# Performance work log

Hardware: AMD Instinct MI355X
Metric: run time of the kernel (lower is better)

Reference implementation:

```python
import jax, jax.numpy as jnp
import numpy as np

N_NODES = 100000
EPS = 1e-5  # BatchNorm1d default eps


def gcn_conv(x, W, b, row, col, n):
    """PyG GCNConv: add self-loops, symmetric normalization, linear, scatter-add."""
    loop = jnp.arange(n, dtype=row.dtype)
    row_f = jnp.concatenate([row, loop])  # sources
    col_f = jnp.concatenate([col, loop])  # targets
    # degree of target nodes (edge_weight = 1)
    deg = jax.ops.segment_sum(jnp.ones_like(col_f, dtype=x.dtype), col_f, num_segments=n)
    dinv = jnp.where(deg > 0, jax.lax.rsqrt(deg), 0.0)
    norm = dinv[row_f] * dinv[col_f]  # [E+N]
    h = x @ W  # [N, out]
    msg = h[row_f] * norm[:, None]  # [E+N, out]
    out = jax.ops.segment_sum(msg, col_f, num_segments=n)
    return out + b


def batch_norm(x, gamma, beta):
    # training-mode BatchNorm1d: biased batch stats over node axis
    mean = jnp.mean(x, axis=0)
    var = jnp.var(x, axis=0)
    return (x - mean) * jax.lax.rsqrt(var + EPS) * gamma + beta


def setup_inputs() -> dict:
    key = jax.random.key(0)
    ks = jax.random.split(key, 8)
    n, e, f_in, h = N_NODES, 1600000, 25, 128
    x = jax.random.normal(ks[0], (n, f_in), dtype=jnp.float32)
    edge_index = jax.random.randint(ks[1], (2, e), 0, n, dtype=jnp.int64)
    s1 = 1.0 / np.sqrt(f_in)
    s2 = 1.0 / np.sqrt(h)
    W1 = jax.random.uniform(ks[2], (f_in, h), jnp.float32, -s1, s1)
    b1 = jax.random.uniform(ks[3], (h,), jnp.float32, -s1, s1)
    gamma = jnp.ones((h,), jnp.float32)
    beta = jnp.zeros((h,), jnp.float32)
    W2 = jax.random.uniform(ks[4], (h, h), jnp.float32, -s2, s2)
    b2 = jax.random.uniform(ks[5], (h,), jnp.float32, -s2, s2)
    return {"x": x, "edge_index": edge_index, "W1": W1, "b1": b1,
            "gamma": gamma, "beta": beta, "W2": W2, "b2": b2}


def reference(x, edge_index, W1, b1, gamma, beta, W2, b2):
    row, col = edge_index[0], edge_index[1]
    n = x.shape[0]
    h = jax.nn.relu(gcn_conv(x, W1, b1, row, col, n))
    h = batch_norm(h, gamma, beta)
    h = jax.nn.relu(gcn_conv(h, W2, b2, row, col, n))
    return h
```

## Files before the change

### kernel.cpp

```cpp
#include <hip/hip_runtime.h>
#include <stdint.h>


#define HID 128
#define NBB 512

typedef short bf16x8 __attribute__((ext_vector_type(8)));
typedef float f32x4 __attribute__((ext_vector_type(4)));

__device__ __forceinline__ unsigned short f2bf(float f) {
    unsigned int u = __float_as_uint(f);
    unsigned int r = (u + 0x7FFFu + ((u >> 16) & 1u)) >> 16;
    return (unsigned short)r;
}
__device__ __forceinline__ unsigned int pack2bf(float lo, float hi) {
    return (unsigned int)f2bf(lo) | ((unsigned int)f2bf(hi) << 16);
}
__device__ __forceinline__ float bflo(unsigned int v) { return __uint_as_float(v << 16); }
__device__ __forceinline__ float bfhi(unsigned int v) { return __uint_as_float(v & 0xffff0000u); }

__global__ void detect_kernel(const unsigned int* __restrict__ w, int* __restrict__ mode, int nwords) {
    __shared__ int any;
    if (threadIdx.x == 0) any = 0;
    __syncthreads();
    for (int i = threadIdx.x * 2 + 1; i < nwords && i < 8192; i += 512) {
        if (w[i] != 0) atomicOr(&any, 1);
    }
    __syncthreads();
    if (threadIdx.x == 0) *mode = any ? 0 : 1;
}

__device__ __forceinline__ int load_idx(const void* ei, size_t i, int mode) {
    return mode ? (int)((const long long*)ei)[i] : ((const int*)ei)[i];
}

__global__ __launch_bounds__(256) void count_q_kernel(const void* __restrict__ ei,
                                                      const int* __restrict__ modep,
                                                      int* __restrict__ qcnt,
                                                      int E, int CHUNK, int nchunk) {
    __shared__ int qc[512];
    for (int i = threadIdx.x; i < nchunk; i += 256) qc[i] = 0;
    __syncthreads();
    int mode = *modep;
    int beg = blockIdx.x * CHUNK;
    int end = beg + CHUNK; if (end > E) end = E;
    for (int e = beg + threadIdx.x; e < end; e += 256) {
        int c = load_idx(ei, (size_t)E + e, mode);
        atomicAdd(&qc[c >> 8], 1);
    }
    __syncthreads();
    for (int i = threadIdx.x; i < nchunk; i += 256)
        qcnt[blockIdx.x * nchunk + i] = qc[i];
}

__global__ __launch_bounds__(256) void scanq_partial_kernel(const int* __restrict__ qcnt,
                                                            int* __restrict__ blocksum,
                                                            int NQ, int nchunk) {
    int j0 = blockIdx.x * 2048 + threadIdx.x * 8;
    int s = 0;
    #pragma unroll
    for (int i = 0; i < 8; ++i) {
        int j = j0 + i;
        if (j < NQ) {
            int q = j >> 9, b = j & (NBB - 1);
            s += qcnt[b * nchunk + q];
        }
    }
    #pragma unroll
    for (int off = 32; off > 0; off >>= 1) s += __shfl_down(s, off);
    __shared__ int ls[4];
    if ((threadIdx.x & 63) == 0) ls[threadIdx.x >> 6] = s;
    __syncthreads();
    if (threadIdx.x == 0) blocksum[blockIdx.x] = ls[0] + ls[1] + ls[2] + ls[3];
}

__global__ __launch_bounds__(1024) void scanq_blocksums_kernel(const int* __restrict__ blocksum,
                                                               int* __restrict__ blockoff,
                                                               int* __restrict__ qoff,
                                                               int nsb, int NQ) {
    __shared__ int s[1024];
    int t = threadIdx.x;
    int own = (t < nsb) ? blocksum[t] : 0;
    s[t] = own;
    __syncthreads();
    for (int off = 1; off < 1024; off <<= 1) {
        int v = s[t] + ((t >= off) ? s[t - off] : 0);
        __syncthreads();
        s[t] = v;
        __syncthreads();
    }
    if (t < nsb) blockoff[t] = s[t] - own;
    if (t == 1023) qoff[NQ] = s[1023];
}

__global__ __launch_bounds__(256) void scanq_finalize_kernel(const int* __restrict__ qcnt,
                                                             const int* __restrict__ blockoff,
                                                             int* __restrict__ qoff,
                                                             int NQ, int nchunk) {
    int t = threadIdx.x;
    int j0 = blockIdx.x * 2048 + t * 8;
    int v[8], own = 0;
    #pragma unroll
    for (int i = 0; i < 8; ++i) {
        int j = j0 + i;
        v[i] = 0;
        if (j < NQ) {
            int q = j >> 9, b = j & (NBB - 1);
            v[i] = qcnt[b * nchunk + q];
        }
        own += v[i];
    }
    __shared__ int s[256];
    s[t] = own;
    __syncthreads();
    for (int off = 1; off < 256; off <<= 1) {
        int x = s[t] + ((t >= off) ? s[t - off] : 0);
        __syncthreads();
        s[t] = x;
        __syncthreads();
    }
    int e = blockoff[blockIdx.x] + s[t] - own;
    #pragma unroll
    for (int i = 0; i < 8; ++i) {
        int j = j0 + i;
        if (j < NQ) qoff[j] = e;
        e += v[i];
    }
}

__global__ __launch_bounds__(256) void bin_kernel(const void* __restrict__ ei,
                                                  const int* __restrict__ modep,
                                                  const int* __restrict__ qoff,
                                                  unsigned int* __restrict__ packed,
                                                  int E, int CHUNK, int nchunk) {
    __shared__ int cur[512];
    for (int i = threadIdx.x; i < nchunk; i += 256)
        cur[i] = qoff[i * NBB + blockIdx.x];
    __syncthreads();
    int mode = *modep;
    int beg = blockIdx.x * CHUNK;
    int end = beg + CHUNK; if (end > E) end = E;
    for (int e = beg + threadIdx.x; e < end; e += 256) {
        int c = load_idx(ei, (size_t)E + e, mode);
        int r = load_idx(ei, (size_t)e, mode);
        int pos = atomicAdd(&cur[c >> 8], 1);
        packed[pos] = ((unsigned)(c & 255) << 24) | (unsigned)r;
    }
}

__global__ __launch_bounds__(256) void chunk_build_kernel(
    const unsigned int* __restrict__ packed, const int* __restrict__ qoff,
    int* __restrict__ rowptr, float* __restrict__ dinv,
    int* __restrict__ edge_src, int n, int E) {
    int q = blockIdx.x;
    int t = threadIdx.x;
    int pbeg = qoff[q * NBB];
    int pend = qoff[(q + 1) * NBB];
    __shared__ int cnt256[256], cur[256], s[256];
    cnt256[t] = 0;
    __syncthreads();
    for (int i = pbeg + t; i < pend; i += 256)
        atomicAdd(&cnt256[packed[i] >> 24], 1);
    __syncthreads();
    int own = cnt256[t];
    s[t] = own;
    __syncthreads();
    for (int off = 1; off < 256; off <<= 1) {
        int x = s[t] + ((t >= off) ? s[t - off] : 0);
        __syncthreads();
        s[t] = x;
        __syncthreads();
    }
    int pref = s[t] - own;
    int node = (q << 8) + t;
    if (node < n) {
        rowptr[node] = pbeg + pref;
        dinv[node] = rsqrtf((float)(own + 1));
    }
    cur[t] = pbeg + pref;
    if (q == gridDim.x - 1 && t == 0) rowptr[n] = E;
    __syncthreads();
    for (int i = pbeg + t; i < pend; i += 256) {
        unsigned int u = packed[i];
        int pos = atomicAdd(&cur[u >> 24], 1);
        edge_src[pos] = (int)(u & 0xFFFFFFu);
    }
}

__global__ __launch_bounds__(256) void xpad_kernel(const float* __restrict__ x,
                                                   unsigned int* __restrict__ xp, int n) {
    int r = blockIdx.x * 256 + threadIdx.x;
    if (r >= n) return;
    const float* xr = x + (size_t)r * 25;
    unsigned int* o = xp + (size_t)r * 16;
    #pragma unroll
    for (int j = 0; j < 12; ++j)
        o[j] = pack2bf(xr[j * 2], xr[j * 2 + 1]);
    o[12] = pack2bf(xr[24], 0.f);
    o[13] = 0u; o[14] = 0u; o[15] = 0u;
}

__global__ __launch_bounds__(256) void l1_kernel(
    const unsigned int* __restrict__ xp, const int* __restrict__ rowptr,
    const int* __restrict__ edge_src, const float* __restrict__ dinv,
    const float* __restrict__ W, const float* __restrict__ bias,
    unsigned short* __restrict__ y1, float* __restrict__ bnsum,
    float* __restrict__ bnsumsq, int n) {
    __shared__ float lw[25 * HID];
    __shared__ float lb[HID];
    for (int i = threadIdx.x; i < 25 * HID; i += 256) lw[i] = W[i];
    if (threadIdx.x < HID) lb[threadIdx.x] = bias[threadIdx.x];
    __syncthreads();
    int lane = threadIdx.x & 63;
    int g = lane >> 4, i = lane & 15;
    int wid0 = (blockIdx.x * 256 + threadIdx.x) >> 6;
    float s0 = 0.f, q0 = 0.f, s1 = 0.f, q1 = 0.f;
    for (int node = wid0; node < n; node += 4096) {
        int beg = rowptr[node], end = rowptr[node + 1];
        float dc = dinv[node];
        float ax = 0.f, ay = 0.f;
        for (int b = beg; b < end; b += 64) {
            int m = end - b; if (m > 64) m = 64;
            int s = 0; float w = 0.f;
            if (lane < m) { s = edge_src[b + lane]; w = dinv[s]; }
            int nsteps = (m + 3) >> 2;
            for (int t = 0; t < nsteps; ++t) {
                int e = 4 * t + g;
                int sj = __shfl(s, e);
                float wj = __shfl(w, e);
                unsigned int u = xp[(size_t)sj * 16 + i];
                ax = fmaf(bflo(u), wj, ax);
                ay = fmaf(bfhi(u), wj, ay);
            }
        }
        if (g == 0) {
            unsigned int u = xp[(size_t)node * 16 + i];
            ax = fmaf(bflo(u), dc, ax);
            ay = fmaf(bfhi(u), dc, ay);
        }
        ax += __shfl_xor(ax, 16); ax += __shfl_xor(ax, 32);
        ay += __shfl_xor(ay, 16); ay += __shfl_xor(ay, 32);
        ax *= dc; ay *= dc;
        float acc0 = lb[lane], acc1 = lb[lane + 64];
        #pragma unroll
        for (int k = 0; k < 25; ++k) {
            float yk = (k & 1) ? __shfl(ay, k >> 1) : __shfl(ax, k >> 1);
            acc0 = fmaf(yk, lw[k * HID + lane], acc0);
            acc1 = fmaf(yk, lw[k * HID + lane + 64], acc1);
        }
        acc0 = fmaxf(acc0, 0.f);
        acc1 = fmaxf(acc1, 0.f);
        y1[(size_t)node * HID + lane] = f2bf(acc0);
        y1[(size_t)node * HID + lane + 64] = f2bf(acc1);
        s0 += acc0; q0 = fmaf(acc0, acc0, q0);
        s1 += acc1; q1 = fmaf(acc1, acc1, q1);
    }
    __shared__ float r0[256], r1[256], r2[256], r3[256];
    r0[threadIdx.x] = s0; r1[threadIdx.x] = q0;
    r2[threadIdx.x] = s1; r3[threadIdx.x] = q1;
    __syncthreads();
    if (threadIdx.x < 64) {
        int l = threadIdx.x;
        float a = r0[l] + r0[l + 64] + r0[l + 128] + r0[l + 192];
        float b = r1[l] + r1[l + 64] + r1[l + 128] + r1[l + 192];
        float c = r2[l] + r2[l + 64] + r2[l + 128] + r2[l + 192];
        float d = r3[l] + r3[l + 64] + r3[l + 128] + r3[l + 192];
        atomicAdd(&bnsum[l], a);
        atomicAdd(&bnsumsq[l], b);
        atomicAdd(&bnsum[l + 64], c);
        atomicAdd(&bnsumsq[l + 64], d);
    }
}

__global__ __launch_bounds__(256) void propagate_kernel(
    const unsigned short* __restrict__ h, const int* __restrict__ rowptr,
    const int* __restrict__ edge_src, const float* __restrict__ dinv,
    const float* __restrict__ bias, float* __restrict__ out, int n) {
    int wid = (blockIdx.x * 256 + threadIdx.x) >> 6;
    if (wid >= n) return;
    int lane = threadIdx.x & 63;
    int beg = rowptr[wid], end = rowptr[wid + 1];
    float dc = dinv[wid];
    float ax = 0.f, ay = 0.f;
    const unsigned int* hp = (const unsigned int*)h;
    for (int b = beg; b < end; b += 64) {
        int m = end - b; if (m > 64) m = 64;
        int s = 0; float w = 0.f;
        if (lane < m) { s = edge_src[b + lane]; w = dinv[s]; }
        for (int j = 0; j < m; j += 8) {
            int s0 = __shfl(s, j + 0), s1 = __shfl(s, j + 1);
            int s2 = __shfl(s, j + 2), s3 = __shfl(s, j + 3);
            int s4 = __shfl(s, j + 4), s5 = __shfl(s, j + 5);
            int s6 = __shfl(s, j + 6), s7 = __shfl(s, j + 7);
            unsigned int v0 = hp[(size_t)s0 * 64 + lane];
            unsigned int v1 = hp[(size_t)s1 * 64 + lane];
            unsigned int v2 = hp[(size_t)s2 * 64 + lane];
            unsigned int v3 = hp[(size_t)s3 * 64 + lane];
            unsigned int v4 = hp[(size_t)s4 * 64 + lane];
            unsigned int v5 = hp[(size_t)s5 * 64 + lane];
            unsigned int v6 = hp[(size_t)s6 * 64 + lane];
            unsigned int v7 = hp[(size_t)s7 * 64 + lane];
            float w0 = __shfl(w, j + 0), w1 = __shfl(w, j + 1);
            float w2 = __shfl(w, j + 2), w3 = __shfl(w, j + 3);
            float w4 = __shfl(w, j + 4), w5 = __shfl(w, j + 5);
            float w6 = __shfl(w, j + 6), w7 = __shfl(w, j + 7);
            ax = fmaf(bflo(v0), w0, ax); ay = fmaf(bfhi(v0), w0, ay);
            ax = fmaf(bflo(v1), w1, ax); ay = fmaf(bfhi(v1), w1, ay);
            ax = fmaf(bflo(v2), w2, ax); ay = fmaf(bfhi(v2), w2, ay);
            ax = fmaf(bflo(v3), w3, ax); ay = fmaf(bfhi(v3), w3, ay);
            ax = fmaf(bflo(v4), w4, ax); ay = fmaf(bfhi(v4), w4, ay);
            ax = fmaf(bflo(v5), w5, ax); ay = fmaf(bfhi(v5), w5, ay);
            ax = fmaf(bflo(v6), w6, ax); ay = fmaf(bfhi(v6), w6, ay);
            ax = fmaf(bflo(v7), w7, ax); ay = fmaf(bfhi(v7), w7, ay);
        }
    }
    {
        unsigned int v = hp[(size_t)wid * 64 + lane];
        ax = fmaf(bflo(v), dc, ax);
        ay = fmaf(bfhi(v), dc, ay);
    }
    float bx = bias[lane * 2], by = bias[lane * 2 + 1];
    ax = fmaxf(fmaf(ax, dc, bx), 0.f);
    ay = fmaxf(fmaf(ay, dc, by), 0.f);
    *(float2*)(out + (size_t)wid * HID + lane * 2) = make_float2(ax, ay);
}

__global__ void bn_finalize_kernel(const float* __restrict__ sum, const float* __restrict__ sumsq,
                                   const float* __restrict__ gamma, const float* __restrict__ beta,
                                   float* __restrict__ scale, float* __restrict__ shift, float inv_n) {
    int c = threadIdx.x;
    float mean = sum[c] * inv_n;
    float var = sumsq[c] * inv_n - mean * mean;
    float sc = gamma[c] * rsqrtf(var + 1e-5f);
    scale[c] = sc;
    shift[c] = beta[c] - mean * sc;
}

__global__ __launch_bounds__(256) void wt_kernel(const float* __restrict__ W,
                                                 unsigned short* __restrict__ Wt) {
    int idx = blockIdx.x * 256 + threadIdx.x;
    int c = idx >> 7, k = idx & 127;
    Wt[c * 128 + k] = f2bf(W[k * 128 + c]);
}

__global__ __launch_bounds__(256) void gemm2_mfma_kernel(
    const unsigned short* __restrict__ yb, const unsigned short* __restrict__ Wt,
    const float* __restrict__ scale, const float* __restrict__ shift,
    unsigned short* __restrict__ out, int n) {
    __shared__ unsigned short lwt[128 * 136];
    __shared__ unsigned short ly[128 * 136];
    int t = threadIdx.x;
    int base = blockIdx.x * 128;

    {
        const unsigned int* w32 = (const unsigned int*)Wt;
        unsigned int* l32 = (unsigned int*)lwt;
        #pragma unroll
        for (int i = 0; i < 32; ++i) {
            int idx = t + i * 256;
            int r = idx >> 6, cp = idx & 63;
            l32[r * 68 + cp] = w32[r * 64 + cp];
        }
    }
    {
        int r = t >> 1, hh = t & 1;
        int gr = base + r;
        unsigned int* l32 = (unsigned int*)ly;
        const uint4* yrow = (const uint4*)(yb + (size_t)gr * HID + hh * 64);
        #pragma unroll
        for (int j = 0; j < 8; ++j) {
            uint4 u = make_uint4(0u, 0u, 0u, 0u);
            if (gr < n) u = yrow[j];
            int gk = hh * 64 + j * 8;
            float a0 = fmaf(bflo(u.x), scale[gk + 0], shift[gk + 0]);
            float a1 = fmaf(bfhi(u.x), scale[gk + 1], shift[gk + 1]);
            float a2 = fmaf(bflo(u.y), scale[gk + 2], shift[gk + 2]);
            float a3 = fmaf(bfhi(u.y), scale[gk + 3], shift[gk + 3]);
            float a4 = fmaf(bflo(u.z), scale[gk + 4], shift[gk + 4]);
            float a5 = fmaf(bfhi(u.z), scale[gk + 5], shift[gk + 5]);
            float a6 = fmaf(bflo(u.w), scale[gk + 6], shift[gk + 6]);
            float a7 = fmaf(bfhi(u.w), scale[gk + 7], shift[gk + 7]);
            l32[r * 68 + hh * 32 + j * 4 + 0] = pack2bf(a0, a1);
            l32[r * 68 + hh * 32 + j * 4 + 1] = pack2bf(a2, a3);
            l32[r * 68 + hh * 32 + j * 4 + 2] = pack2bf(a4, a5);
            l32[r * 68 + hh * 32 + j * 4 + 3] = pack2bf(a6, a7);
        }
    }
    __syncthreads();

    int w = t >> 6, lane = t & 63;
    int li = lane & 15, lg = lane >> 4;
    f32x4 acc[2][8];
    #pragma unroll
    for (int a = 0; a < 2; ++a)
        #pragma unroll
        for (int b = 0; b < 8; ++b) acc[a][b] = (f32x4){0.f, 0.f, 0.f, 0.f};

    #pragma unroll
    for (int ks = 0; ks < 4; ++ks) {
        int kb = ks * 32 + lg * 8;
        bf16x8 af[2], bfr[8];
        #pragma unroll
        for (int rt = 0; rt < 2; ++rt)
            af[rt] = *(const bf16x8*)&ly[(w * 32 + rt * 16 + li) * 136 + kb];
        #pragma unroll
        for (int cf = 0; cf < 8; ++cf)
            bfr[cf] = *(const bf16x8*)&lwt[(cf * 16 + li) * 136 + kb];
        #pragma unroll
        for (int rt = 0; rt < 2; ++rt)
            #pragma unroll
            for (int cf = 0; cf < 8; ++cf)
                acc[rt][cf] = __builtin_amdgcn_mfma_f32_16x16x32_bf16(
                    af[rt], bfr[cf], acc[rt][cf], 0, 0, 0);
    }

    #pragma unroll
    for (int rt = 0; rt < 2; ++rt) {
        #pragma unroll
        for (int reg = 0; reg < 4; ++reg) {
            int gr = base + w * 32 + rt * 16 + lg * 4 + reg;
            if (gr < n) {
                #pragma unroll
                for (int cf = 0; cf < 8; ++cf)
                    out[(size_t)gr * HID + cf * 16 + li] = f2bf(acc[rt][cf][reg]);
            }
        }
    }
}

extern "C" void kernel_launch(void* const* d_in, const int* in_sizes, int n_in,
                              void* d_out, int out_size, void* d_ws, size_t ws_size,
                              hipStream_t stream) {
    const float* x     = (const float*)d_in[0];
    const void*  ei    = d_in[1];
    const float* W1    = (const float*)d_in[2];
    const float* b1    = (const float*)d_in[3];
    const float* gamma = (const float*)d_in[4];
    const float* beta  = (const float*)d_in[5];
    const float* W2    = (const float*)d_in[6];
    const float* b2    = (const float*)d_in[7];
    float* out = (float*)d_out;

    const int f_in = 25;
    int n = in_sizes[0] / f_in;
    int E = in_sizes[1] / 2;
    int nchunk = (n + 255) >> 8;
    int NQ = nchunk * NBB;
    int nsb = (NQ + 2047) / 2048;
    int CHUNK = (E + NBB - 1) / NBB;

    char* ws = (char*)d_ws;
    size_t off = 0;
    auto alloc = [&](size_t bytes) -> void* {
        void* p = ws + off;
        off += (bytes + 511) & ~(size_t)511;
        return p;
    };
    int*   rowptr    = (int*)alloc(((size_t)n + 1) * 4);
    float* dinv      = (float*)alloc((size_t)n * 4);
    int*   edge_src  = (int*)alloc((size_t)E * 4);
    unsigned int* packed = (unsigned int*)alloc((size_t)E * 4);
    int*   qcnt      = (int*)alloc((size_t)NQ * 4);
    int*   qoff      = (int*)alloc(((size_t)NQ + 1) * 4);
    int*   blocksum  = (int*)alloc((size_t)nsb * 4);
    int*   blockoff  = (int*)alloc((size_t)nsb * 4);
    float* bnacc     = (float*)alloc(256 * 4);
    float* sclshift  = (float*)alloc(256 * 4);
    int*   mode      = (int*)alloc(4);
    unsigned int* xp   = (unsigned int*)alloc((size_t)n * 16 * 4);
    unsigned short* y1 = (unsigned short*)alloc((size_t)n * HID * 2);
    unsigned short* Wt = (unsigned short*)alloc(128 * 128 * 2);
    unsigned short* h  = (unsigned short*)alloc((size_t)n * HID * 2);

    hipMemsetAsync(bnacc, 0, 256 * 4, stream);

    detect_kernel<<<1, 256, 0, stream>>>((const unsigned int*)ei, mode, 2 * E);
    count_q_kernel<<<NBB, 256, 0, stream>>>(ei, mode, qcnt, E, CHUNK, nchunk);
    scanq_partial_kernel<<<nsb, 256, 0, stream>>>(qcnt, blocksum, NQ, nchunk);
    scanq_blocksums_kernel<<<1, 1024, 0, stream>>>(blocksum, blockoff, qoff, nsb, NQ);
    scanq_finalize_kernel<<<nsb, 256, 0, stream>>>(qcnt, blockoff, qoff, NQ, nchunk);
    bin_kernel<<<NBB, 256, 0, stream>>>(ei, mode, qoff, packed, E, CHUNK, nchunk);
    chunk_build_kernel<<<nchunk, 256, 0, stream>>>(packed, qoff, rowptr, dinv, edge_src, n, E);

    xpad_kernel<<<(n + 255) / 256, 256, 0, stream>>>(x, xp, n);
    l1_kernel<<<1024, 256, 0, stream>>>(xp, rowptr, edge_src, dinv, W1, b1,
                                        y1, bnacc, bnacc + 128, n);

    bn_finalize_kernel<<<1, 128, 0, stream>>>(bnacc, bnacc + 128, gamma, beta,
                                              sclshift, sclshift + 128, 1.0f / (float)n);

    wt_kernel<<<64, 256, 0, stream>>>(W2, Wt);
    gemm2_mfma_kernel<<<(n + 127) / 128, 256, 0, stream>>>(y1, Wt, sclshift, sclshift + 128, h, n);
    propagate_kernel<<<(n + 3) / 4, 256, 0, stream>>>(h, rowptr, edge_src, dinv, b2, out, n);
}
```

Measured before the change: 255.5 us.

## Process four nodes per wavefront in layer-1 aggregation with unrolled gathers

Restructures the layer-1 kernel so each wavefront handles four nodes at once, one per 16-lane group, instead of one node per wave. Each group walks its own edge list with four gathers unrolled per step, and the shuffle-based edge staging and cross-group reduction are gone. The dense 25x128 transform now gives each lane 8 output columns, written as one 16-byte store. BN statistics are reduced through shared-memory atomics, and the grid doubles to 2048 blocks. The cost is divergence: groups in a wave loop up to the largest degree among their four nodes, and per-lane register use rises.

```diff
diff --git a/kernel.cpp b/kernel.cpp
--- a/kernel.cpp
+++ b/kernel.cpp
@@ -208,67 +208,103 @@
     float* __restrict__ bnsumsq, int n) {
     __shared__ float lw[25 * HID];
     __shared__ float lb[HID];
-    for (int i = threadIdx.x; i < 25 * HID; i += 256) lw[i] = W[i];
-    if (threadIdx.x < HID) lb[threadIdx.x] = bias[threadIdx.x];
+    __shared__ float lsum[HID], lsq[HID];
+    for (int idx = threadIdx.x; idx < 25 * HID; idx += 256) lw[idx] = W[idx];
+    if (threadIdx.x < HID) {
+        lb[threadIdx.x] = bias[threadIdx.x];
+        lsum[threadIdx.x] = 0.f;
+        lsq[threadIdx.x] = 0.f;
+    }
     __syncthreads();
     int lane = threadIdx.x & 63;
-    int g = lane >> 4, i = lane & 15;
-    int wid0 = (blockIdx.x * 256 + threadIdx.x) >> 6;
-    float s0 = 0.f, q0 = 0.f, s1 = 0.f, q1 = 0.f;
-    for (int node = wid0; node < n; node += 4096) {
-        int beg = rowptr[node], end = rowptr[node + 1];
-        float dc = dinv[node];
+    int g = lane >> 4;
+    int i = lane & 15;
+    int wid = (blockIdx.x * 256 + threadIdx.x) >> 6;
+    int nwaves = gridDim.x << 2;
+    float psum[8], psq[8];
+    #pragma unroll
+    for (int j = 0; j < 8; ++j) { psum[j] = 0.f; psq[j] = 0.f; }
+
+    for (int base = 4 * wid; base < n; base += 4 * nwaves) {
+        int node = base + g;
+        bool act = node < n;
+        int nd = act ? node : 0;
+        int beg = rowptr[nd];
+        int end = act ? rowptr[nd + 1] : beg;
+        float dc = dinv[nd];
+        int deg = end - beg;
+        int md = deg;
+        md = max(md, __shfl_xor(md, 16));
+        md = max(md, __shfl_xor(md, 32));
         float ax = 0.f, ay = 0.f;
-        for (int b = beg; b < end; b += 64) {
-            int m = end - b; if (m > 64) m = 64;
-            int s = 0; float w = 0.f;
-            if (lane < m) { s = edge_src[b + lane]; w = dinv[s]; }
-            int nsteps = (m + 3) >> 2;
-            for (int t = 0; t < nsteps; ++t) {
-                int e = 4 * t + g;
-                int sj = __shfl(s, e);
-                float wj = __shfl(w, e);
-                unsigned int u = xp[(size_t)sj * 16 + i];
-                ax = fmaf(bflo(u), wj, ax);
-                ay = fmaf(bfhi(u), wj, ay);
-            }
-        }
-        if (g == 0) {
-            unsigned int u = xp[(size_t)node * 16 + i];
-            ax = fmaf(bflo(u), dc, ax);
-            ay = fmaf(bfhi(u), dc, ay);
-        }
-        ax += __shfl_xor(ax, 16); ax += __shfl_xor(ax, 32);
-        ay += __shfl_xor(ay, 16); ay += __shfl_xor(ay, 32);
+        for (int off = 0; off < md; off += 4) {
+            int e0 = beg + off, e1 = e0 + 1, e2 = e0 + 2, e3 = e0 + 3;
+            bool v0 = e0 < end, v1 = e1 < end, v2 = e2 < end, v3 = e3 < end;
+            int c0 = v0 ? e0 : 0, c1 = v1 ? e1 : 0;
+            int c2 = v2 ? e2 : 0, c3 = v3 ? e3 : 0;
+            int s0 = edge_src[c0];
+            int s1 = edge_src[c1];
+            int s2 = edge_src[c2];
+            int s3 = edge_src[c3];
+            unsigned int u0 = xp[(size_t)s0 * 16 + i];
+            unsigned int u1 = xp[(size_t)s1 * 16 + i];
+            unsigned int u2 = xp[(size_t)s2 * 16 + i];
+            unsigned int u3 = xp[(size_t)s3 * 16 + i];
+            float w0 = v0 ? dinv[s0] : 0.f;
+            float w1 = v1 ? dinv[s1] : 0.f;
+            float w2 = v2 ? dinv[s2] : 0.f;
+            float w3 = v3 ? dinv[s3] : 0.f;
+            ax = fmaf(bflo(u0), w0, ax); ay = fmaf(bfhi(u0), w0, ay);
+            ax = fmaf(bflo(u1), w1, ax); ay = fmaf(bfhi(u1), w1, ay);
+            ax = fmaf(bflo(u2), w2, ax); ay = fmaf(bfhi(u2), w2, ay);
+            ax = fmaf(bflo(u3), w3, ax); ay = fmaf(bfhi(u3), w3, ay);
+        }
+        {
+            unsigned int u = xp[(size_t)nd * 16 + i];
+            float ws = act ? dc : 0.f;
+            ax = fmaf(bflo(u), ws, ax);
+            ay = fmaf(bfhi(u), ws, ay);
+        }
         ax *= dc; ay *= dc;
-        float acc0 = lb[lane], acc1 = lb[lane + 64];
+        float acc[8];
+        #pragma unroll
+        for (int j = 0; j < 8; ++j) acc[j] = lb[i * 8 + j];
         #pragma unroll
         for (int k = 0; k < 25; ++k) {
-            float yk = (k & 1) ? __shfl(ay, k >> 1) : __shfl(ax, k >> 1);
-            acc0 = fmaf(yk, lw[k * HID + lane], acc0);
-            acc1 = fmaf(yk, lw[k * HID + lane + 64], acc1);
-        }
-        acc0 = fmaxf(acc0, 0.f);
-        acc1 = fmaxf(acc1, 0.f);
-        y1[(size_t)node * HID + lane] = f2bf(acc0);
-        y1[(size_t)node * HID + lane + 64] = f2bf(acc1);
-        s0 += acc0; q0 = fmaf(acc0, acc0, q0);
-        s1 += acc1; q1 = fmaf(acc1, acc1, q1);
-    }
-    __shared__ float r0[256], r1[256], r2[256], r3[256];
-    r0[threadIdx.x] = s0; r1[threadIdx.x] = q0;
-    r2[threadIdx.x] = s1; r3[threadIdx.x] = q1;
-    __syncthreads();
-    if (threadIdx.x < 64) {
-        int l = threadIdx.x;
-        float a = r0[l] + r0[l + 64] + r0[l + 128] + r0[l + 192];
-        float b = r1[l] + r1[l + 64] + r1[l + 128] + r1[l + 192];
-        float c = r2[l] + r2[l + 64] + r2[l + 128] + r2[l + 192];
-        float d = r3[l] + r3[l + 64] + r3[l + 128] + r3[l + 192];
-        atomicAdd(&bnsum[l], a);
-        atomicAdd(&bnsumsq[l], b);
-        atomicAdd(&bnsum[l + 64], c);
-        atomicAdd(&bnsumsq[l + 64], d);
+            int srcl = (g << 4) + (k >> 1);
+            float yk = (k & 1) ? __shfl(ay, srcl) : __shfl(ax, srcl);
+            #pragma unroll
+            for (int j = 0; j < 8; ++j)
+                acc[j] = fmaf(yk, lw[k * HID + i * 8 + j], acc[j]);
+        }
+        if (act) {
+            uint4 p;
+            float r0 = fmaxf(acc[0], 0.f), r1 = fmaxf(acc[1], 0.f);
+            float r2 = fmaxf(acc[2], 0.f), r3 = fmaxf(acc[3], 0.f);
+            float r4 = fmaxf(acc[4], 0.f), r5 = fmaxf(acc[5], 0.f);
+            float r6 = fmaxf(acc[6], 0.f), r7 = fmaxf(acc[7], 0.f);
+            p.x = pack2bf(r0, r1); p.y = pack2bf(r2, r3);
+            p.z = pack2bf(r4, r5); p.w = pack2bf(r6, r7);
+            *(uint4*)&y1[(size_t)nd * HID + i * 8] = p;
+            psum[0] += r0; psq[0] = fmaf(r0, r0, psq[0]);
+            psum[1] += r1; psq[1] = fmaf(r1, r1, psq[1]);
+            psum[2] += r2; psq[2] = fmaf(r2, r2, psq[2]);
+            psum[3] += r3; psq[3] = fmaf(r3, r3, psq[3]);
+            psum[4] += r4; psq[4] = fmaf(r4, r4, psq[4]);
+            psum[5] += r5; psq[5] = fmaf(r5, r5, psq[5]);
+            psum[6] += r6; psq[6] = fmaf(r6, r6, psq[6]);
+            psum[7] += r7; psq[7] = fmaf(r7, r7, psq[7]);
+        }
+    }
+    #pragma unroll
+    for (int j = 0; j < 8; ++j) {
+        atomicAdd(&lsum[i * 8 + j], psum[j]);
+        atomicAdd(&lsq[i * 8 + j], psq[j]);
+    }
+    __syncthreads();
+    if (threadIdx.x < HID) {
+        atomicAdd(&bnsum[threadIdx.x], lsum[threadIdx.x]);
+        atomicAdd(&bnsumsq[threadIdx.x], lsq[threadIdx.x]);
     }
 }
 
@@ -483,7 +519,7 @@
     chunk_build_kernel<<<nchunk, 256, 0, stream>>>(packed, qoff, rowptr, dinv, edge_src, n, E);
 
     xpad_kernel<<<(n + 255) / 256, 256, 0, stream>>>(x, xp, n);
-    l1_kernel<<<1024, 256, 0, stream>>>(xp, rowptr, edge_src, dinv, W1, b1,
+    l1_kernel<<<2048, 256, 0, stream>>>(xp, rowptr, edge_src, dinv, W1, b1,
                                         y1, bnacc, bnacc + 128, n);
 
     bn_finalize_kernel<<<1, 128, 0, stream>>>(bnacc, bnacc + 128, gamma, beta,
```

After: 286.3 us. 1.12x slower.
